# Optimization experiments

Hardware: AMD Instinct MI355X
Metric: run time of the kernel (lower is better)

The kernel has to match this reference:

```python
import jax, jax.numpy as jnp
import numpy as np

V, NJ, NCOMP, NBETA = 778, 16, 24, 10
F_CLOSED, N_ANCHOR = 1554, 32
B, NOBJ = 8, 16384
# MANO kinematic tree parents (wrist + 5 fingers x 3 joints)
PARENTS = np.array([-1, 0, 1, 2, 0, 4, 5, 0, 7, 8, 0, 10, 11, 0, 13, 14])


def setup_inputs() -> dict:
    key = jax.random.key(0)
    ks = jax.random.split(key, 12)
    hand_pose = jax.random.normal(ks[0], (B, 3 + 3 + NCOMP), jnp.float32) * 0.1
    obj_points = jax.random.normal(ks[1], (B, NOBJ, 3), jnp.float32) * 0.1
    hand_beta = jax.random.normal(ks[2], (B, NBETA), jnp.float32) * 0.5
    v_template = jax.random.normal(ks[3], (V, 3), jnp.float32) * 0.05
    shapedirs = jax.random.normal(ks[4], (V, 3, NBETA), jnp.float32) * 0.01
    posedirs = jax.random.normal(ks[5], (V, 3, (NJ - 1) * 9), jnp.float32) * 0.01
    J_regressor = jax.nn.softmax(jax.random.normal(ks[6], (NJ, V), jnp.float32), axis=-1)
    lbs_weights = jax.nn.softmax(jax.random.normal(ks[7], (V, NJ), jnp.float32) * 2.0, axis=-1)
    pca_comps = jax.random.normal(ks[8], (NCOMP, (NJ - 1) * 3), jnp.float32) * 0.1
    anchor_weights = jax.nn.softmax(jax.random.normal(ks[9], (N_ANCHOR, 3), jnp.float32), axis=-1)
    closed_faces = jax.random.randint(ks[10], (F_CLOSED, 3), 0, V, jnp.int32)
    anchor_face_idx = jax.random.randint(ks[11], (N_ANCHOR, 3), 0, V, jnp.int32)
    return dict(hand_pose=hand_pose, obj_points=obj_points, hand_beta=hand_beta,
                v_template=v_template, shapedirs=shapedirs, posedirs=posedirs,
                J_regressor=J_regressor, lbs_weights=lbs_weights, pca_comps=pca_comps,
                anchor_weights=anchor_weights, closed_faces=closed_faces,
                anchor_face_idx=anchor_face_idx)


def rodrigues(r):
    # r: [..., 3] axis-angle -> [..., 3, 3] rotation matrix
    theta = jnp.sqrt(jnp.sum(r * r, axis=-1, keepdims=True) + 1e-16)
    k = r / theta
    c = jnp.cos(theta)[..., None]
    s = jnp.sin(theta)[..., None]
    kx, ky, kz = k[..., 0], k[..., 1], k[..., 2]
    zero = jnp.zeros_like(kx)
    K = jnp.stack([zero, -kz, ky, kz, zero, -kx, -ky, kx, zero], axis=-1)
    K = K.reshape(r.shape[:-1] + (3, 3))
    I = jnp.eye(3, dtype=r.dtype)
    return c * I + s * K + (1.0 - c) * k[..., :, None] * k[..., None, :]


def mano_verts(hand_pose, hand_beta, v_template, shapedirs, posedirs,
               J_regressor, lbs_weights, pca_comps):
    b = hand_pose.shape[0]
    trans = hand_pose[:, :3]
    root = hand_pose[:, 3:6]
    hand45 = hand_pose[:, 6:] @ pca_comps  # PCA -> 45-dim pose (flat_hand_mean: no mean add)
    full = jnp.concatenate([root, hand45], axis=-1).reshape(b, NJ, 3)
    R = rodrigues(full)  # [B,16,3,3]
    v_shaped = v_template + jnp.einsum('vdk,bk->bvd', shapedirs, hand_beta)
    J = jnp.einsum('jv,bvd->bjd', J_regressor, v_shaped)  # [B,16,3]
    pose_feat = (R[:, 1:] - jnp.eye(3, dtype=R.dtype)).reshape(b, (NJ - 1) * 9)
    v_posed = v_shaped + jnp.einsum('vdp,bp->bvd', posedirs, pose_feat)

    def make44(Rj, tj):  # [B,3,3],[B,3] -> [B,4,4]
        T = jnp.zeros((b, 4, 4), R.dtype)
        return T.at[:, :3, :3].set(Rj).at[:, :3, 3].set(tj).at[:, 3, 3].set(1.0)

    Ts = [make44(R[:, 0], J[:, 0])]
    for j in range(1, NJ):  # fixed small kinematic chain
        p = int(PARENTS[j])
        Ts.append(jnp.einsum('bmn,bnk->bmk', Ts[p], make44(R[:, j], J[:, j] - J[:, p])))
    T = jnp.stack(Ts, axis=1)  # [B,16,4,4] global joint transforms
    corr = jnp.einsum('bjmn,bjn->bjm', T[..., :3, :3], J)
    A = T.at[..., :3, 3].add(-corr)  # relative-to-rest transforms
    Tw = jnp.einsum('vj,bjmn->bvmn', lbs_weights, A)  # per-vertex skinning transform
    verts = jnp.einsum('bvmn,bvn->bvm', Tw[..., :3, :3], v_posed) + Tw[..., :3, 3]
    return verts + trans[:, None, :]


def vertex_normals(verts, faces):  # verts [B,V,3], faces [F,3]
    def one(v):
        p0, p1, p2 = v[faces[:, 0]], v[faces[:, 1]], v[faces[:, 2]]
        fn = jnp.cross(p1 - p0, p2 - p0)
        vn = (jnp.zeros_like(v).at[faces[:, 0]].add(fn)
              .at[faces[:, 1]].add(fn).at[faces[:, 2]].add(fn))
        return vn / (jnp.linalg.norm(vn, axis=-1, keepdims=True) + 1e-8)
    return jax.vmap(one)(verts)


def reference(hand_pose, obj_points, hand_beta, v_template, shapedirs, posedirs,
              J_regressor, lbs_weights, pca_comps, anchor_weights,
              closed_faces, anchor_face_idx):
    verts = mano_verts(hand_pose, hand_beta, v_template, shapedirs, posedirs,
                       J_regressor, lbs_weights, pca_comps)  # [B,778,3]
    # get_NN: squared cdist obj->hand + argmin (the memory-bound bottleneck)
    d2 = (jnp.sum(obj_points * obj_points, -1, keepdims=True)
          + jnp.sum(verts * verts, -1)[:, None, :]
          - 2.0 * jnp.einsum('bnd,bvd->bnv', obj_points, verts))  # [B,NOBJ,778]
    nn_idx = jnp.argmin(d2, axis=-1)  # [B,NOBJ]
    nn_dist = jnp.take_along_axis(d2, nn_idx[..., None], axis=-1)[..., 0]
    # contact_map_of_m_to_n
    cmap = 1.0 - 2.0 * (jax.nn.sigmoid(100.0 * nn_dist) - 0.5)
    # inter_penetr_loss: interior obj points (behind nearest hand vertex normal)
    normals = vertex_normals(verts, closed_faces)
    nn_vert = jnp.take_along_axis(verts, nn_idx[..., None], axis=1)
    nn_norm = jnp.take_along_axis(normals, nn_idx[..., None], axis=1)
    interior = jnp.sum((nn_vert - obj_points) * nn_norm, axis=-1) > 0.0
    penetration = jnp.sum(jnp.where(interior, nn_dist, 0.0)) / hand_pose.shape[0]
    # AnchorLayer: barycentric anchor points on the hand surface
    contact_candidates = jnp.einsum('ak,bakd->bad', anchor_weights, verts[:, anchor_face_idx])
    return cmap, penetration, verts, contact_candidates
```

## Files before the change

kernel.cpp:

```cpp
#include <hip/hip_runtime.h>
#include <math.h>

#define NV 778
#define NVP 780
#define NJ 16
#define NCOMP 24
#define NBETA 10
#define FC 1554
#define NA 32
#define NB 8
#define NOBJ 16384
#define VD (NV*3)
#define BCH 584

__global__ __launch_bounds__(256) void k_blend(
    const float* __restrict__ hp, const float* __restrict__ pca,
    const float* __restrict__ vt, const float* __restrict__ sd,
    const float* __restrict__ pd, const float* __restrict__ beta,
    float* __restrict__ VS, float* __restrict__ VP,
    float* __restrict__ sRg, float* __restrict__ pen)
{
    int b = blockIdx.x / BCH, c = blockIdx.x % BCH;
    int t = threadIdx.x;
    int wid = t >> 6, lane = t & 63;
    __shared__ float h45[45];
    __shared__ float sR[NJ*9];
    __shared__ float spf[135];

    if (t < 45) {
        float acc = 0.0f;
        #pragma unroll
        for (int k = 0; k < NCOMP; ++k) acc += hp[b*30 + 6 + k] * pca[k*45 + t];
        h45[t] = acc;
    }
    __syncthreads();
    if (t < NJ) {
        float rx, ry, rz;
        if (t == 0) { rx = hp[b*30+3]; ry = hp[b*30+4]; rz = hp[b*30+5]; }
        else        { rx = h45[(t-1)*3]; ry = h45[(t-1)*3+1]; rz = h45[(t-1)*3+2]; }
        float th = sqrtf(rx*rx + ry*ry + rz*rz + 1e-16f);
        float kx = rx/th, ky = ry/th, kz = rz/th;
        float cc = cosf(th), s = sinf(th), o = 1.0f - cc;
        float R[9];
        R[0] = cc + o*kx*kx;     R[1] = -s*kz + o*kx*ky;  R[2] =  s*ky + o*kx*kz;
        R[3] =  s*kz + o*ky*kx;  R[4] = cc + o*ky*ky;     R[5] = -s*kx + o*ky*kz;
        R[6] = -s*ky + o*kz*kx;  R[7] =  s*kx + o*kz*ky;  R[8] = cc + o*kz*kz;
        #pragma unroll
        for (int i = 0; i < 9; ++i) sR[t*9+i] = R[i];
        if (c == 0) {
            #pragma unroll
            for (int i = 0; i < 9; ++i) sRg[b*(NJ*9) + t*9 + i] = R[i];
        }
    }
    __syncthreads();
    if (t < 135) {
        int mn = t % 9;
        float d = (mn == 0 || mn == 4 || mn == 8) ? 1.0f : 0.0f;
        spf[t] = sR[9 + t] - d;
    }
    if (b == 0 && c == 0 && t == 0) *pen = 0.0f;
    __syncthreads();

    int r = c*4 + wid;
    if (r < VD) {
        const float* p  = pd + r * 135;
        float accP = p[lane] * spf[lane] + p[lane+64] * spf[lane+64];
        accP += (lane < 7) ? p[lane+128] * spf[lane+128] : 0.0f;

        float accS = (lane < NBETA) ? sd[r*NBETA + lane] * beta[b*NBETA + lane] : 0.0f;

        #pragma unroll
        for (int off = 32; off; off >>= 1) {
            accP += __shfl_down(accP, off, 64);
            accS += __shfl_down(accS, off, 64);
        }
        if (lane == 0) {
            float vs = vt[r] + accS;
            VS[b*VD + r] = vs;
            VP[b*VD + r] = vs + accP;
        }
    }
}

__global__ __launch_bounds__(1024) void k_skel(
    const float* __restrict__ hp, const float* __restrict__ sRg,
    const float* __restrict__ Jreg, const float* __restrict__ VS,
    const float* __restrict__ VP, const float* __restrict__ W,
    const int* __restrict__ faces, const float* __restrict__ aw,
    const int* __restrict__ afi,
    float* __restrict__ verts, float4* __restrict__ PK,
    float* __restrict__ NRM, float* __restrict__ contact)
{
    int b = blockIdx.x, t = threadIdx.x;
    int lane = t & 63, wid = t >> 6;
    __shared__ float sR[NJ*9];
    __shared__ float sJ[NJ*3];
    __shared__ float4 sA4[NJ*3];
    __shared__ float sv[VD];
    __shared__ float sn[VD];

    if (t < NJ*9) sR[t] = sRg[b*NJ*9 + t];
    if (t < 2) PK[b*NVP + NV + t] = make_float4(0.f, 0.f, 0.f, 1e30f);
    for (int i = t; i < VD; i += 1024) sn[i] = 0.0f;

    {
        float a0 = 0.0f, a1 = 0.0f, a2 = 0.0f;
        for (int v = lane; v < NV; v += 64) {
            const float* p = VS + b*VD + v*3;
            float w = Jreg[wid*NV + v];
            a0 += w*p[0]; a1 += w*p[1]; a2 += w*p[2];
        }
        #pragma unroll
        for (int off = 32; off; off >>= 1) {
            a0 += __shfl_down(a0, off, 64);
            a1 += __shfl_down(a1, off, 64);
            a2 += __shfl_down(a2, off, 64);
        }
        if (lane == 0) {
            sJ[wid*3+0] = a0; sJ[wid*3+1] = a1; sJ[wid*3+2] = a2;
        }
    }
    __syncthreads();

    if (t < 3) {
        const int par[NJ] = {-1,0,1,2,0,4,5,0,7,8,0,10,11,0,13,14};
        int m = t;
        float Tr[NJ][3], Tt[NJ];
        Tr[0][0] = sR[m*3+0]; Tr[0][1] = sR[m*3+1]; Tr[0][2] = sR[m*3+2];
        Tt[0] = sJ[m];
        #pragma unroll
        for (int j = 1; j < NJ; ++j) {
            int p = par[j];
            float t0 = sJ[j*3+0] - sJ[p*3+0];
            float t1 = sJ[j*3+1] - sJ[p*3+1];
            float t2 = sJ[j*3+2] - sJ[p*3+2];
            float a0 = Tr[p][0], a1 = Tr[p][1], a2 = Tr[p][2];
            #pragma unroll
            for (int n = 0; n < 3; ++n)
                Tr[j][n] = a0*sR[j*9+n] + a1*sR[j*9+3+n] + a2*sR[j*9+6+n];
            Tt[j] = a0*t0 + a1*t1 + a2*t2 + Tt[p];
        }
        #pragma unroll
        for (int j = 0; j < NJ; ++j) {
            float corr = Tr[j][0]*sJ[j*3] + Tr[j][1]*sJ[j*3+1] + Tr[j][2]*sJ[j*3+2];
            sA4[j*3 + m] = make_float4(Tr[j][0], Tr[j][1], Tr[j][2], Tt[j] - corr);
        }
    }
    __syncthreads();

    float tx = hp[b*30+0], ty = hp[b*30+1], tz = hp[b*30+2];
    for (int v = t; v < NV; v += 1024) {
        float4 r0 = make_float4(0,0,0,0), r1 = make_float4(0,0,0,0), r2 = make_float4(0,0,0,0);
        const float* w = W + v * NJ;
        for (int j = 0; j < NJ; ++j) {
            float wj = w[j];
            float4 A0 = sA4[j*3+0], A1 = sA4[j*3+1], A2 = sA4[j*3+2];
            r0.x += wj*A0.x; r0.y += wj*A0.y; r0.z += wj*A0.z; r0.w += wj*A0.w;
            r1.x += wj*A1.x; r1.y += wj*A1.y; r1.z += wj*A1.z; r1.w += wj*A1.w;
            r2.x += wj*A2.x; r2.y += wj*A2.y; r2.z += wj*A2.z; r2.w += wj*A2.w;
        }
        int i = b*NV + v;
        float px = VP[b*VD + v*3], py = VP[b*VD + v*3+1], pz = VP[b*VD + v*3+2];
        float x = r0.x*px + r0.y*py + r0.z*pz + r0.w + tx;
        float y = r1.x*px + r1.y*py + r1.z*pz + r1.w + ty;
        float z = r2.x*px + r2.y*py + r2.z*pz + r2.w + tz;
        sv[v*3] = x; sv[v*3+1] = y; sv[v*3+2] = z;
        verts[i*3] = x; verts[i*3+1] = y; verts[i*3+2] = z;
        PK[b*NVP + v] = make_float4(x, y, z, 0.5f*(x*x + y*y + z*z));
    }
    __syncthreads();

    for (int f = t; f < FC; f += 1024) {
        int i0 = faces[f*3], i1 = faces[f*3+1], i2 = faces[f*3+2];
        float ax = sv[i1*3+0]-sv[i0*3+0], ay = sv[i1*3+1]-sv[i0*3+1], az = sv[i1*3+2]-sv[i0*3+2];
        float bx = sv[i2*3+0]-sv[i0*3+0], by = sv[i2*3+1]-sv[i0*3+1], bz = sv[i2*3+2]-sv[i0*3+2];
        float cx = ay*bz - az*by, cy = az*bx - ax*bz, cz = ax*by - ay*bx;
        atomicAdd(&sn[i0*3+0], cx); atomicAdd(&sn[i0*3+1], cy); atomicAdd(&sn[i0*3+2], cz);
        atomicAdd(&sn[i1*3+0], cx); atomicAdd(&sn[i1*3+1], cy); atomicAdd(&sn[i1*3+2], cz);
        atomicAdd(&sn[i2*3+0], cx); atomicAdd(&sn[i2*3+1], cy); atomicAdd(&sn[i2*3+2], cz);
    }
    __syncthreads();

    for (int i = t; i < VD; i += 1024) NRM[b*VD + i] = sn[i];
    if (t < NA*3) {
        int a = t / 3, d = t % 3;
        float acc = 0.0f;
        #pragma unroll
        for (int k = 0; k < 3; ++k)
            acc += aw[a*3 + k] * sv[afi[a*3 + k]*3 + d];
        contact[b*NA*3 + t] = acc;
    }
}

__global__ __launch_bounds__(256) void k_nn(const float* __restrict__ obj,
                                            const float4* __restrict__ PK,
                                            const float* __restrict__ NRM,
                                            float* __restrict__ cmap,
                                            float* __restrict__ pen)
{
    int t = threadIdx.x, lane = t & 63;
    int b = blockIdx.x >> 5;
    int n0 = (blockIdx.x & 31) * 512 + t;
    int n1 = n0 + 256;
    int base = b * NV;

    __shared__ float4 sPK[NVP];
    for (int i = t; i < NVP; i += 256) sPK[i] = PK[b*NVP + i];
    __syncthreads();

    const float* o0 = obj + (b*NOBJ + n0)*3;
    const float* o1 = obj + (b*NOBJ + n1)*3;
    float ox0 = o0[0], oy0 = o0[1], oz0 = o0[2];
    float ox1 = o1[0], oy1 = o1[1], oz1 = o1[2];

    float sA0 = 1e30f, sB0 = 1e30f, sA1 = 1e30f, sB1 = 1e30f;
    int   jA0 = 0,     jB0 = 390,   jA1 = 0,     jB1 = 390;
    #pragma unroll 2
    for (int j = 0; j < 390; ++j) {
        float4 va = sPK[j];
        float4 vb = sPK[j + 390];
        {
            float s = fmaf(-ox0, va.x, va.w); s = fmaf(-oy0, va.y, s); s = fmaf(-oz0, va.z, s);
            if (s < sA0) { sA0 = s; jA0 = j; }
        }
        {
            float s = fmaf(-ox0, vb.x, vb.w); s = fmaf(-oy0, vb.y, s); s = fmaf(-oz0, vb.z, s);
            if (s < sB0) { sB0 = s; jB0 = j + 390; }
        }
        {
            float s = fmaf(-ox1, va.x, va.w); s = fmaf(-oy1, va.y, s); s = fmaf(-oz1, va.z, s);
            if (s < sA1) { sA1 = s; jA1 = j; }
        }
        {
            float s = fmaf(-ox1, vb.x, vb.w); s = fmaf(-oy1, vb.y, s); s = fmaf(-oz1, vb.z, s);
            if (s < sB1) { sB1 = s; jB1 = j + 390; }
        }
    }
    if (sB0 < sA0) { sA0 = sB0; jA0 = jB0; }
    if (sB1 < sA1) { sA1 = sB1; jA1 = jB1; }

    float osq0 = ox0*ox0 + oy0*oy0 + oz0*oz0;
    float d20 = 2.0f * sA0 + osq0;
    cmap[b*NOBJ + n0] = 2.0f / (1.0f + __expf(100.0f * d20));
    float4 q0 = sPK[jA0];
    float nx0 = NRM[(base + jA0)*3 + 0];
    float ny0 = NRM[(base + jA0)*3 + 1];
    float nz0 = NRM[(base + jA0)*3 + 2];
    float dp0 = (q0.x - ox0)*nx0 + (q0.y - oy0)*ny0 + (q0.z - oz0)*nz0;
    float p = (dp0 > 0.0f) ? d20 : 0.0f;

    float osq1 = ox1*ox1 + oy1*oy1 + oz1*oz1;
    float d21 = 2.0f * sA1 + osq1;
    cmap[b*NOBJ + n1] = 2.0f / (1.0f + __expf(100.0f * d21));
    float4 q1 = sPK[jA1];
    float nx1 = NRM[(base + jA1)*3 + 0];
    float ny1 = NRM[(base + jA1)*3 + 1];
    float nz1 = NRM[(base + jA1)*3 + 2];
    float dp1 = (q1.x - ox1)*nx1 + (q1.y - oy1)*ny1 + (q1.z - oz1)*nz1;
    p += (dp1 > 0.0f) ? d21 : 0.0f;

    for (int off = 32; off; off >>= 1) p += __shfl_down(p, off, 64);
    __shared__ float wsum[4];
    if (lane == 0) wsum[t >> 6] = p;
    __syncthreads();
    if (t == 0) atomicAdd(pen, (wsum[0] + wsum[1] + wsum[2] + wsum[3]) * (1.0f / NB));
}

extern "C" void kernel_launch(void* const* d_in, const int* in_sizes, int n_in,
                              void* d_out, int out_size, void* d_ws, size_t ws_size,
                              hipStream_t stream)
{
    const float* hp    = (const float*)d_in[0];
    const float* obj   = (const float*)d_in[1];
    const float* beta  = (const float*)d_in[2];
    const float* vt    = (const float*)d_in[3];
    const float* sd    = (const float*)d_in[4];
    const float* pd    = (const float*)d_in[5];
    const float* Jreg  = (const float*)d_in[6];
    const float* W     = (const float*)d_in[7];
    const float* pca   = (const float*)d_in[8];
    const float* aw    = (const float*)d_in[9];
    const int*   faces = (const int*)d_in[10];
    const int*   afi   = (const int*)d_in[11];

    float* out     = (float*)d_out;
    float* cmap    = out;
    float* pen     = out + NB*NOBJ;
    float* verts   = out + NB*NOBJ + 1;
    float* contact = out + NB*NOBJ + 1 + NB*NV*3;

    float* ws   = (float*)d_ws;
    float4* PK  = (float4*)ws;
    float* NRM  = ws + NB*NVP*4;
    float* VS   = NRM + NB*VD;
    float* VP   = VS + NB*VD;
    float* sRg  = VP + NB*VD;

    k_blend<<<NB*BCH, 256, 0, stream>>>(hp, pca, vt, sd, pd, beta, VS, VP, sRg, pen);
    k_skel <<<NB, 1024, 0, stream>>>(hp, sRg, Jreg, VS, VP, W, faces, aw, afi,
                                     verts, PK, NRM, contact);
    k_nn   <<<NB*32, 256, 0, stream>>>(obj, PK, NRM, cmap, pen);
}
```

Baseline: 147.8 us.

## Fuse skeleton/skinning/normals into the nearest-neighbour kernel, recomputed per block

```diff
diff --git a/kernel.cpp b/kernel.cpp
--- a/kernel.cpp
+++ b/kernel.cpp
@@ -2,7 +2,6 @@
 #include <math.h>
 
 #define NV 778
-#define NVP 780
 #define NJ 16
 #define NCOMP 24
 #define NBETA 10
@@ -12,13 +11,14 @@
 #define NOBJ 16384
 #define VD (NV*3)
 #define BCH 584
+#define CH 392
+#define NVL 792
 
 __global__ __launch_bounds__(256) void k_blend(
     const float* __restrict__ hp, const float* __restrict__ pca,
     const float* __restrict__ vt, const float* __restrict__ sd,
     const float* __restrict__ pd, const float* __restrict__ beta,
-    float* __restrict__ VS, float* __restrict__ VP,
-    float* __restrict__ sRg, float* __restrict__ pen)
+    float* __restrict__ VS, float* __restrict__ VP, float* __restrict__ pen)
 {
     int b = blockIdx.x / BCH, c = blockIdx.x % BCH;
     int t = threadIdx.x;
@@ -47,10 +47,6 @@
         R[6] = -s*ky + o*kz*kx;  R[7] =  s*kx + o*kz*ky;  R[8] = cc + o*kz*kz;
         #pragma unroll
         for (int i = 0; i < 9; ++i) sR[t*9+i] = R[i];
-        if (c == 0) {
-            #pragma unroll
-            for (int i = 0; i < 9; ++i) sRg[b*(NJ*9) + t*9 + i] = R[i];
-        }
     }
     __syncthreads();
     if (t < 135) {
@@ -82,42 +78,77 @@
     }
 }
 
-__global__ __launch_bounds__(1024) void k_skel(
-    const float* __restrict__ hp, const float* __restrict__ sRg,
+__global__ __launch_bounds__(256) void k_mega(
+    const float* __restrict__ hp, const float* __restrict__ pca,
     const float* __restrict__ Jreg, const float* __restrict__ VS,
     const float* __restrict__ VP, const float* __restrict__ W,
     const int* __restrict__ faces, const float* __restrict__ aw,
-    const int* __restrict__ afi,
-    float* __restrict__ verts, float4* __restrict__ PK,
-    float* __restrict__ NRM, float* __restrict__ contact)
+    const int* __restrict__ afi, const float* __restrict__ obj,
+    float* __restrict__ verts, float* __restrict__ cmap,
+    float* __restrict__ contact, float* __restrict__ pen)
 {
-    int b = blockIdx.x, t = threadIdx.x;
-    int lane = t & 63, wid = t >> 6;
+    int blk = blockIdx.x;
+    int b = blk >> 5;
+    int g = blk & 31;
+    int t = threadIdx.x, lane = t & 63, wid = t >> 6;
+
+    __shared__ float4 sPK[NVL];
+    __shared__ float sv[VD];
+    __shared__ float sn[VD];
     __shared__ float sR[NJ*9];
     __shared__ float sJ[NJ*3];
     __shared__ float4 sA4[NJ*3];
-    __shared__ float sv[VD];
-    __shared__ float sn[VD];
-
-    if (t < NJ*9) sR[t] = sRg[b*NJ*9 + t];
-    if (t < 2) PK[b*NVP + NV + t] = make_float4(0.f, 0.f, 0.f, 1e30f);
-    for (int i = t; i < VD; i += 1024) sn[i] = 0.0f;
+    __shared__ float h45[45];
+    __shared__ float wsum[4];
+
+    int n0 = g*512 + t;
+    int n1 = n0 + 256;
+    const float* o0p = obj + (b*NOBJ + n0)*3;
+    const float* o1p = obj + (b*NOBJ + n1)*3;
+    float ox0 = o0p[0], oy0 = o0p[1], oz0 = o0p[2];
+    float ox1 = o1p[0], oy1 = o1p[1], oz1 = o1p[2];
+
+    if (t < 45) {
+        float acc = 0.0f;
+        #pragma unroll
+        for (int k = 0; k < NCOMP; ++k) acc += hp[b*30 + 6 + k] * pca[k*45 + t];
+        h45[t] = acc;
+    }
+    for (int i = t; i < VD; i += 256) sn[i] = 0.0f;
+    if (t < NVL - NV) sPK[NV + t] = make_float4(0.f, 0.f, 0.f, 1e30f);
+    __syncthreads();
+    if (t < NJ) {
+        float rx, ry, rz;
+        if (t == 0) { rx = hp[b*30+3]; ry = hp[b*30+4]; rz = hp[b*30+5]; }
+        else        { rx = h45[(t-1)*3]; ry = h45[(t-1)*3+1]; rz = h45[(t-1)*3+2]; }
+        float th = sqrtf(rx*rx + ry*ry + rz*rz + 1e-16f);
+        float kx = rx/th, ky = ry/th, kz = rz/th;
+        float cc = cosf(th), s = sinf(th), o = 1.0f - cc;
+        sR[t*9+0] = cc + o*kx*kx;     sR[t*9+1] = -s*kz + o*kx*ky;  sR[t*9+2] =  s*ky + o*kx*kz;
+        sR[t*9+3] =  s*kz + o*ky*kx;  sR[t*9+4] = cc + o*ky*ky;     sR[t*9+5] = -s*kx + o*ky*kz;
+        sR[t*9+6] = -s*ky + o*kz*kx;  sR[t*9+7] =  s*kx + o*kz*ky;  sR[t*9+8] = cc + o*kz*kz;
+    }
+    __syncthreads();
 
     {
-        float a0 = 0.0f, a1 = 0.0f, a2 = 0.0f;
+        float ac[12];
+        #pragma unroll
+        for (int q = 0; q < 12; ++q) ac[q] = 0.0f;
         for (int v = lane; v < NV; v += 64) {
             const float* p = VS + b*VD + v*3;
-            float w = Jreg[wid*NV + v];
-            a0 += w*p[0]; a1 += w*p[1]; a2 += w*p[2];
-        }
-        #pragma unroll
-        for (int off = 32; off; off >>= 1) {
-            a0 += __shfl_down(a0, off, 64);
-            a1 += __shfl_down(a1, off, 64);
-            a2 += __shfl_down(a2, off, 64);
-        }
+            float x = p[0], y = p[1], z = p[2];
+            #pragma unroll
+            for (int jj = 0; jj < 4; ++jj) {
+                float w = Jreg[(4*wid + jj)*NV + v];
+                ac[jj*3+0] += w*x; ac[jj*3+1] += w*y; ac[jj*3+2] += w*z;
+            }
+        }
+        #pragma unroll
+        for (int q = 0; q < 12; ++q)
+            for (int off = 32; off; off >>= 1) ac[q] += __shfl_down(ac[q], off, 64);
         if (lane == 0) {
-            sJ[wid*3+0] = a0; sJ[wid*3+1] = a1; sJ[wid*3+2] = a2;
+            #pragma unroll
+            for (int q = 0; q < 12; ++q) sJ[(4*wid + q/3)*3 + (q%3)] = ac[q];
         }
     }
     __syncthreads();
@@ -149,7 +180,7 @@
     __syncthreads();
 
     float tx = hp[b*30+0], ty = hp[b*30+1], tz = hp[b*30+2];
-    for (int v = t; v < NV; v += 1024) {
+    for (int v = t; v < NV; v += 256) {
         float4 r0 = make_float4(0,0,0,0), r1 = make_float4(0,0,0,0), r2 = make_float4(0,0,0,0);
         const float* w = W + v * NJ;
         for (int j = 0; j < NJ; ++j) {
@@ -159,18 +190,20 @@
             r1.x += wj*A1.x; r1.y += wj*A1.y; r1.z += wj*A1.z; r1.w += wj*A1.w;
             r2.x += wj*A2.x; r2.y += wj*A2.y; r2.z += wj*A2.z; r2.w += wj*A2.w;
         }
-        int i = b*NV + v;
         float px = VP[b*VD + v*3], py = VP[b*VD + v*3+1], pz = VP[b*VD + v*3+2];
         float x = r0.x*px + r0.y*py + r0.z*pz + r0.w + tx;
         float y = r1.x*px + r1.y*py + r1.z*pz + r1.w + ty;
         float z = r2.x*px + r2.y*py + r2.z*pz + r2.w + tz;
         sv[v*3] = x; sv[v*3+1] = y; sv[v*3+2] = z;
-        verts[i*3] = x; verts[i*3+1] = y; verts[i*3+2] = z;
-        PK[b*NVP + v] = make_float4(x, y, z, 0.5f*(x*x + y*y + z*z));
-    }
-    __syncthreads();
-
-    for (int f = t; f < FC; f += 1024) {
+        sPK[v] = make_float4(x, y, z, 0.5f*(x*x + y*y + z*z));
+        if (g == 0) {
+            int i = b*NV + v;
+            verts[i*3] = x; verts[i*3+1] = y; verts[i*3+2] = z;
+        }
+    }
+    __syncthreads();
+
+    for (int f = t; f < FC; f += 256) {
         int i0 = faces[f*3], i1 = faces[f*3+1], i2 = faces[f*3+2];
         float ax = sv[i1*3+0]-sv[i0*3+0], ay = sv[i1*3+1]-sv[i0*3+1], az = sv[i1*3+2]-sv[i0*3+2];
         float bx = sv[i2*3+0]-sv[i0*3+0], by = sv[i2*3+1]-sv[i0*3+1], bz = sv[i2*3+2]-sv[i0*3+2];
@@ -181,8 +214,7 @@
     }
     __syncthreads();
 
-    for (int i = t; i < VD; i += 1024) NRM[b*VD + i] = sn[i];
-    if (t < NA*3) {
+    if (g == 0 && t < NA*3) {
         int a = t / 3, d = t % 3;
         float acc = 0.0f;
         #pragma unroll
@@ -190,51 +222,33 @@
             acc += aw[a*3 + k] * sv[afi[a*3 + k]*3 + d];
         contact[b*NA*3 + t] = acc;
     }
-}
-
-__global__ __launch_bounds__(256) void k_nn(const float* __restrict__ obj,
-                                            const float4* __restrict__ PK,
-                                            const float* __restrict__ NRM,
-                                            float* __restrict__ cmap,
-                                            float* __restrict__ pen)
-{
-    int t = threadIdx.x, lane = t & 63;
-    int b = blockIdx.x >> 5;
-    int n0 = (blockIdx.x & 31) * 512 + t;
-    int n1 = n0 + 256;
-    int base = b * NV;
-
-    __shared__ float4 sPK[NVP];
-    for (int i = t; i < NVP; i += 256) sPK[i] = PK[b*NVP + i];
-    __syncthreads();
-
-    const float* o0 = obj + (b*NOBJ + n0)*3;
-    const float* o1 = obj + (b*NOBJ + n1)*3;
-    float ox0 = o0[0], oy0 = o0[1], oz0 = o0[2];
-    float ox1 = o1[0], oy1 = o1[1], oz1 = o1[2];
 
     float sA0 = 1e30f, sB0 = 1e30f, sA1 = 1e30f, sB1 = 1e30f;
-    int   jA0 = 0,     jB0 = 390,   jA1 = 0,     jB1 = 390;
+    int   jA0 = 0,     jB0 = CH,    jA1 = 0,     jB1 = CH;
+
+    float4 a0 = sPK[0],  b0 = sPK[CH];
+    float4 a1 = sPK[1],  b1 = sPK[CH+1];
     #pragma unroll 2
-    for (int j = 0; j < 390; ++j) {
-        float4 va = sPK[j];
-        float4 vb = sPK[j + 390];
+    for (int j = 0; j < CH; ++j) {
+        float4 a2 = sPK[j+2];
+        float4 b2 = sPK[j+CH+2];
         {
-            float s = fmaf(-ox0, va.x, va.w); s = fmaf(-oy0, va.y, s); s = fmaf(-oz0, va.z, s);
+            float s = fmaf(-ox0, a0.x, a0.w); s = fmaf(-oy0, a0.y, s); s = fmaf(-oz0, a0.z, s);
             if (s < sA0) { sA0 = s; jA0 = j; }
         }
         {
-            float s = fmaf(-ox0, vb.x, vb.w); s = fmaf(-oy0, vb.y, s); s = fmaf(-oz0, vb.z, s);
-            if (s < sB0) { sB0 = s; jB0 = j + 390; }
+            float s = fmaf(-ox0, b0.x, b0.w); s = fmaf(-oy0, b0.y, s); s = fmaf(-oz0, b0.z, s);
+            if (s < sB0) { sB0 = s; jB0 = j + CH; }
         }
         {
-            float s = fmaf(-ox1, va.x, va.w); s = fmaf(-oy1, va.y, s); s = fmaf(-oz1, va.z, s);
+            float s = fmaf(-ox1, a0.x, a0.w); s = fmaf(-oy1, a0.y, s); s = fmaf(-oz1, a0.z, s);
             if (s < sA1) { sA1 = s; jA1 = j; }
         }
         {
-            float s = fmaf(-ox1, vb.x, vb.w); s = fmaf(-oy1, vb.y, s); s = fmaf(-oz1, vb.z, s);
-            if (s < sB1) { sB1 = s; jB1 = j + 390; }
-        }
+            float s = fmaf(-ox1, b0.x, b0.w); s = fmaf(-oy1, b0.y, s); s = fmaf(-oz1, b0.z, s);
+            if (s < sB1) { sB1 = s; jB1 = j + CH; }
+        }
+        a0 = a1; b0 = b1; a1 = a2; b1 = b2;
     }
     if (sB0 < sA0) { sA0 = sB0; jA0 = jB0; }
     if (sB1 < sA1) { sA1 = sB1; jA1 = jB1; }
@@ -243,25 +257,18 @@
     float d20 = 2.0f * sA0 + osq0;
     cmap[b*NOBJ + n0] = 2.0f / (1.0f + __expf(100.0f * d20));
     float4 q0 = sPK[jA0];
-    float nx0 = NRM[(base + jA0)*3 + 0];
-    float ny0 = NRM[(base + jA0)*3 + 1];
-    float nz0 = NRM[(base + jA0)*3 + 2];
-    float dp0 = (q0.x - ox0)*nx0 + (q0.y - oy0)*ny0 + (q0.z - oz0)*nz0;
+    float dp0 = (q0.x - ox0)*sn[jA0*3+0] + (q0.y - oy0)*sn[jA0*3+1] + (q0.z - oz0)*sn[jA0*3+2];
     float p = (dp0 > 0.0f) ? d20 : 0.0f;
 
     float osq1 = ox1*ox1 + oy1*oy1 + oz1*oz1;
     float d21 = 2.0f * sA1 + osq1;
     cmap[b*NOBJ + n1] = 2.0f / (1.0f + __expf(100.0f * d21));
     float4 q1 = sPK[jA1];
-    float nx1 = NRM[(base + jA1)*3 + 0];
-    float ny1 = NRM[(base + jA1)*3 + 1];
-    float nz1 = NRM[(base + jA1)*3 + 2];
-    float dp1 = (q1.x - ox1)*nx1 + (q1.y - oy1)*ny1 + (q1.z - oz1)*nz1;
+    float dp1 = (q1.x - ox1)*sn[jA1*3+0] + (q1.y - oy1)*sn[jA1*3+1] + (q1.z - oz1)*sn[jA1*3+2];
     p += (dp1 > 0.0f) ? d21 : 0.0f;
 
     for (int off = 32; off; off >>= 1) p += __shfl_down(p, off, 64);
-    __shared__ float wsum[4];
-    if (lane == 0) wsum[t >> 6] = p;
+    if (lane == 0) wsum[wid] = p;
     __syncthreads();
     if (t == 0) atomicAdd(pen, (wsum[0] + wsum[1] + wsum[2] + wsum[3]) * (1.0f / NB));
 }
@@ -290,14 +297,10 @@
     float* contact = out + NB*NOBJ + 1 + NB*NV*3;
 
     float* ws   = (float*)d_ws;
-    float4* PK  = (float4*)ws;
-    float* NRM  = ws + NB*NVP*4;
-    float* VS   = NRM + NB*VD;
+    float* VS   = ws;
     float* VP   = VS + NB*VD;
-    float* sRg  = VP + NB*VD;
-
-    k_blend<<<NB*BCH, 256, 0, stream>>>(hp, pca, vt, sd, pd, beta, VS, VP, sRg, pen);
-    k_skel <<<NB, 1024, 0, stream>>>(hp, sRg, Jreg, VS, VP, W, faces, aw, afi,
-                                     verts, PK, NRM, contact);
-    k_nn   <<<NB*32, 256, 0, stream>>>(obj, PK, NRM, cmap, pen);
+
+    k_blend<<<NB*BCH, 256, 0, stream>>>(hp, pca, vt, sd, pd, beta, VS, VP, pen);
+    k_mega <<<NB*32, 256, 0, stream>>>(hp, pca, Jreg, VS, VP, W, faces, aw, afi,
+                                       obj, verts, cmap, contact, pen);
 }
```

After: 146.5 us. Within noise of the previous version (-0.9%).
